# Kernel tuning notes

Measured on AMD Instinct MI355X. Metric: run time of the kernel, lower is better.

Reference implementation:

```python
import jax, jax.numpy as jnp
import numpy as np

BASE_DIM = 512
NUM_HEADS = 4
HEAD_DIM = BASE_DIM // NUM_HEADS
NUM_USERS = 100000
TIMESLOTS = 24
B, S = 64, 512


def setup_inputs() -> dict:
    key = jax.random.key(0)
    ks = jax.random.split(key, 16)
    timeslot_embedded = jax.random.normal(ks[0], (TIMESLOTS, BASE_DIM), jnp.float32)
    smoothed_timeslot_embedded = jax.random.normal(ks[1], (TIMESLOTS, BASE_DIM), jnp.float32)
    user_embedded = jax.random.normal(ks[2], (B, BASE_DIM), jnp.float32)
    user_x = jax.random.randint(ks[3], (B,), 0, NUM_USERS)
    hour_x = jax.random.randint(ks[4], (B, S), 0, TIMESLOTS)
    hour_mask = jax.random.randint(ks[5], (B, S, TIMESLOTS), 0, 2)
    # guarantee no row is fully masked (avoids all -inf softmax rows)
    hour_mask = hour_mask.at[:, :, 0].set(0)
    sc = 0.02
    user_pref_table = jax.random.normal(ks[6], (NUM_USERS, BASE_DIM), jnp.float32) * sc
    Wq = jax.random.normal(ks[7], (NUM_HEADS, HEAD_DIM, 2 * BASE_DIM), jnp.float32) * sc
    bq = jnp.zeros((NUM_HEADS, HEAD_DIM), jnp.float32)
    Wk = jax.random.normal(ks[8], (NUM_HEADS, HEAD_DIM, BASE_DIM), jnp.float32) * sc
    bk = jnp.zeros((NUM_HEADS, HEAD_DIM), jnp.float32)
    Wv = jax.random.normal(ks[9], (NUM_HEADS, HEAD_DIM, BASE_DIM), jnp.float32) * sc
    bv = jnp.zeros((NUM_HEADS, HEAD_DIM), jnp.float32)
    W_unify = jax.random.normal(ks[10], (BASE_DIM, BASE_DIM), jnp.float32) * sc
    b_unify = jnp.zeros((BASE_DIM,), jnp.float32)
    W_time = jax.random.normal(ks[11], (TIMESLOTS, BASE_DIM), jnp.float32) * sc
    b_time = jnp.zeros((TIMESLOTS,), jnp.float32)
    return dict(timeslot_embedded=timeslot_embedded,
                smoothed_timeslot_embedded=smoothed_timeslot_embedded,
                user_embedded=user_embedded,
                user_x=user_x, hour_x=hour_x, hour_mask=hour_mask,
                user_pref_table=user_pref_table,
                Wq=Wq, bq=bq, Wk=Wk, bk=bk, Wv=Wv, bv=bv,
                W_unify=W_unify, b_unify=b_unify,
                W_time=W_time, b_time=b_time)


def reference(timeslot_embedded, smoothed_timeslot_embedded, user_embedded,
              user_x, hour_x, hour_mask, user_pref_table,
              Wq, bq, Wk, bk, Wv, bv, W_unify, b_unify, W_time, b_time):
    b, s = hour_x.shape
    n = b * s
    hour = hour_x.reshape(n)                                  # [N]
    mask = hour_mask.reshape(n, TIMESLOTS)                    # [N, 24]

    # user preference broadcast over sequence, then flattened
    up = user_pref_table[user_x]                              # [B, D]
    user_feature = jnp.broadcast_to(up[:, None, :], (b, s, BASE_DIM)).reshape(n, BASE_DIM)
    time_feature = timeslot_embedded[hour]                    # [N, D]
    query = jnp.concatenate([user_feature, time_feature], axis=-1)  # [N, 2D]

    # all heads batched (equivalent to the per-head Python loop + concat)
    q = jnp.einsum('nd,hed->nhe', query, Wq) + bq             # [N, H, E]
    k = jnp.einsum('kd,hed->khe', timeslot_embedded, Wk) + bk # [24, H, E]
    v = jnp.einsum('kd,hed->khe', timeslot_embedded, Wv) + bv # [24, H, E]

    scale = 1.0 / jnp.sqrt(jnp.float32(HEAD_DIM))
    scores = jnp.einsum('nhe,khe->nhk', q, k) * scale         # [N, H, 24]
    scores = jnp.where(mask[:, None, :] == 1, -jnp.inf, scores)
    attn = jax.nn.softmax(scores, axis=-1)
    out = jnp.einsum('nhk,khe->nhe', attn, v).reshape(n, BASE_DIM)  # concat heads

    head_outputs = out.reshape(b, s, BASE_DIM)
    at_emb = head_outputs @ W_unify.T + b_unify               # [B, S, D]
    time_logits = head_outputs @ W_time.T + b_time            # [B, S, 24]
    return at_emb, time_logits
```

## Files before the change

### kernel.cpp

```cpp
#include <hip/hip_runtime.h>
#include <hip/hip_bf16.h>
#include <math.h>

#define TS   24
#define NH   4
#define HD   128
#define D    512
#define NB   64
#define SEQ  512
#define NTOT (NB*SEQ)

typedef __bf16 bf16;
typedef __bf16 bf16x8 __attribute__((ext_vector_type(8)));
typedef float  f32x4  __attribute__((ext_vector_type(4)));

#define OFF_QU  0
#define OFF_QT  32768
#define OFF_K   45056
#define OFF_V   57344
#define OFF_SU  69632
#define OFF_ST  75776
#define OFF_BSW 78080

__global__ __launch_bounds__(256) void k1_proj(
    const float* __restrict__ timeslot, const int* __restrict__ user_x,
    const float* __restrict__ upt,
    const float* __restrict__ Wq, const float* __restrict__ bq,
    const float* __restrict__ Wk, const float* __restrict__ bk,
    const float* __restrict__ Wv, const float* __restrict__ bv,
    float* __restrict__ ws)
{
    int tau = blockIdx.x * 256 + threadIdx.x;
    if (tau < 32768) {
        int he = tau >> 6, b = tau & 63;
        const float4* wrow = (const float4*)(Wq + (size_t)he * 1024);
        int u = user_x[b];
        const float4* urow = (const float4*)(upt + (size_t)u * 512);
        float acc = bq[he];
        #pragma unroll 4
        for (int d = 0; d < 128; ++d) {
            float4 w = wrow[d], x = urow[d];
            acc += w.x*x.x + w.y*x.y + w.z*x.z + w.w*x.w;
        }
        ws[OFF_QU + b*512 + he] = acc;
    } else if (tau < 69632) {
        int idx = tau - 32768;
        int sec = idx / 12288;
        int r   = idx % 12288;
        int he  = r / 24, t = r % 24;
        const float* wbase; float bias; int outoff;
        if (sec == 0)      { wbase = Wq + (size_t)he*1024 + 512; bias = 0.f;    outoff = OFF_QT; }
        else if (sec == 1) { wbase = Wk + (size_t)he*512;        bias = bk[he]; outoff = OFF_K;  }
        else               { wbase = Wv + (size_t)he*512;        bias = bv[he]; outoff = OFF_V;  }
        const float4* w4 = (const float4*)wbase;
        const float4* x4 = (const float4*)(timeslot + t*512);
        float acc = bias;
        #pragma unroll 4
        for (int d = 0; d < 128; ++d) {
            float4 w = w4[d], x = x4[d];
            acc += w.x*x.x + w.y*x.y + w.z*x.z + w.w*x.w;
        }
        ws[outoff + t*512 + he] = acc;
    }
}

static __device__ __forceinline__ float dot128(const float* __restrict__ a,
                                               const float* __restrict__ b) {
    const float4* a4 = (const float4*)a;
    const float4* b4 = (const float4*)b;
    float acc = 0.f;
    #pragma unroll 8
    for (int i = 0; i < 32; ++i) {
        float4 x = a4[i], y = b4[i];
        acc += x.x*y.x + x.y*y.y + x.z*y.z + x.w*y.w;
    }
    return acc;
}

__global__ __launch_bounds__(256) void k2_small(
    const float* __restrict__ Wu, const float* __restrict__ Wt,
    float* __restrict__ ws)
{
    const float SCL = 1.4426950408889634f / sqrtf(128.0f);
    int tau = blockIdx.x * 256 + threadIdx.x;
    bf16* Bsw = (bf16*)(ws + OFF_BSW);
    if (tau < 6144) {
        int kk = tau % 24, h = (tau / 24) & 3, b = tau / 96;
        float acc = dot128(ws + OFF_QU + b*512 + h*128, ws + OFF_K + kk*512 + h*128);
        ws[OFF_SU + tau] = acc * SCL;
    } else if (tau < 8448) {
        int i = tau - 6144;
        int kk = i % 24, h = (i / 24) & 3, t = i / 96;
        float acc = dot128(ws + OFF_QT + t*512 + h*128, ws + OFF_K + kk*512 + h*128);
        ws[OFF_ST + i] = acc * SCL;
    } else if (tau < 57600) {
        int i = tau - 8448;
        int c = i & 511, r96 = i >> 9;
        int h = r96 / 24, kk = r96 % 24;
        float acc = dot128(ws + OFF_V + kk*512 + h*128, Wu + (size_t)c*512 + h*128);
        Bsw[((r96 >> 3)*544 + c)*8 + (r96 & 7)] = (bf16)acc;
    } else if (tau < 59904) {
        int i = tau - 57600;
        int j = i % 24, r96 = i / 24;
        int h = r96 / 24, kk = r96 % 24;
        float acc = dot128(ws + OFF_V + kk*512 + h*128, Wt + (size_t)j*512 + h*128);
        Bsw[((r96 >> 3)*544 + 512 + j)*8 + (r96 & 7)] = (bf16)acc;
    } else if (tau < 60672) {
        int i = tau - 59904;
        int g = i >> 6, rem = i & 63;
        int c = 536 + (rem >> 3), j = rem & 7;
        Bsw[(g*544 + c)*8 + j] = (bf16)0.f;
    }
}

__global__ __launch_bounds__(256) void k3_main(
    const int* __restrict__ hour_x, const int* __restrict__ hour_mask,
    const float* __restrict__ b_unify, const float* __restrict__ b_time,
    const float* __restrict__ ws, float* __restrict__ out)
{
    __shared__ int  maskL[128 * 24];
    __shared__ int  hourL[128];
    __shared__ __align__(16) bf16 attnL[128][104];

    int tid = threadIdx.x;
    int n0  = blockIdx.x * 128;
    int b   = n0 >> 9;

    {
        const int4* src = (const int4*)(hour_mask + (size_t)n0 * 24);
        int4* dst = (int4*)maskL;
        #pragma unroll
        for (int i = tid; i < 128 * 24 / 4; i += 256)
            dst[i] = src[i];
        if (tid < 128) hourL[tid] = hour_x[n0 + tid];
    }
    __syncthreads();

    #pragma unroll
    for (int it = 0; it < 2; ++it) {
        int task = tid + it * 256;
        int h = task >> 7, row = task & 127;
        int t = hourL[row];
        const float* su = ws + OFF_SU + (b*4 + h)*24;
        const float* st = ws + OFF_ST + (t*4 + h)*24;
        const int*   m  = maskL + row*24;
        float w[24]; float sum = 0.f;
        #pragma unroll
        for (int kk = 0; kk < 24; ++kk) {
            float e = exp2f(su[kk] + st[kk]);
            e = m[kk] ? 0.f : e;
            w[kk] = e; sum += e;
        }
        float inv = 1.f / sum;
        #pragma unroll
        for (int kk = 0; kk < 24; ++kk)
            attnL[row][h*24 + kk] = (bf16)(w[kk] * inv);
    }
    __syncthreads();

    const bf16* Bsw = (const bf16*)(ws + OFF_BSW);
    int wv = tid >> 6, l = tid & 63;
    int quad = l >> 4, cl = l & 15;
    int r0 = wv*32 + cl;
    int r1 = r0 + 16;

    bf16x8 a00 = *(const bf16x8*)&attnL[r0][ 0 + quad*8];
    bf16x8 a01 = *(const bf16x8*)&attnL[r0][32 + quad*8];
    bf16x8 a02 = *(const bf16x8*)&attnL[r0][64 + quad*8];
    bf16x8 a10 = *(const bf16x8*)&attnL[r1][ 0 + quad*8];
    bf16x8 a11 = *(const bf16x8*)&attnL[r1][32 + quad*8];
    bf16x8 a12 = *(const bf16x8*)&attnL[r1][64 + quad*8];

    int nbase = n0 + wv*32 + quad*4;

    for (int ct = 0; ct < 32; ++ct) {
        int col = ct*16 + cl;
        const bf16* bp = Bsw + ((size_t)(quad*544 + col)) * 8;
        bf16x8 b0 = *(const bf16x8*)(bp);
        bf16x8 b1 = *(const bf16x8*)(bp + 4*544*8);
        bf16x8 b2 = *(const bf16x8*)(bp + 8*544*8);
        f32x4 acc0 = {0.f, 0.f, 0.f, 0.f};
        f32x4 acc1 = {0.f, 0.f, 0.f, 0.f};
        acc0 = __builtin_amdgcn_mfma_f32_16x16x32_bf16(a00, b0, acc0, 0, 0, 0);
        acc1 = __builtin_amdgcn_mfma_f32_16x16x32_bf16(a10, b0, acc1, 0, 0, 0);
        acc0 = __builtin_amdgcn_mfma_f32_16x16x32_bf16(a01, b1, acc0, 0, 0, 0);
        acc1 = __builtin_amdgcn_mfma_f32_16x16x32_bf16(a11, b1, acc1, 0, 0, 0);
        acc0 = __builtin_amdgcn_mfma_f32_16x16x32_bf16(a02, b2, acc0, 0, 0, 0);
        acc1 = __builtin_amdgcn_mfma_f32_16x16x32_bf16(a12, b2, acc1, 0, 0, 0);
        float bias = b_unify[col];
        #pragma unroll
        for (int r = 0; r < 4; ++r) {
            out[(size_t)(nbase + r)*512 + col]      = acc0[r] + bias;
            out[(size_t)(nbase + 16 + r)*512 + col] = acc1[r] + bias;
        }
    }

    float* tl_out = out + (size_t)NTOT * 512;
    for (int ct = 32; ct < 34; ++ct) {
        int col = ct*16 + cl;
        int cc  = col - 512;
        const bf16* bp = Bsw + ((size_t)(quad*544 + col)) * 8;
        bf16x8 b0 = *(const bf16x8*)(bp);
        bf16x8 b1 = *(const bf16x8*)(bp + 4*544*8);
        bf16x8 b2 = *(const bf16x8*)(bp + 8*544*8);
        f32x4 acc0 = {0.f, 0.f, 0.f, 0.f};
        f32x4 acc1 = {0.f, 0.f, 0.f, 0.f};
        acc0 = __builtin_amdgcn_mfma_f32_16x16x32_bf16(a00, b0, acc0, 0, 0, 0);
        acc1 = __builtin_amdgcn_mfma_f32_16x16x32_bf16(a10, b0, acc1, 0, 0, 0);
        acc0 = __builtin_amdgcn_mfma_f32_16x16x32_bf16(a01, b1, acc0, 0, 0, 0);
        acc1 = __builtin_amdgcn_mfma_f32_16x16x32_bf16(a11, b1, acc1, 0, 0, 0);
        acc0 = __builtin_amdgcn_mfma_f32_16x16x32_bf16(a02, b2, acc0, 0, 0, 0);
        acc1 = __builtin_amdgcn_mfma_f32_16x16x32_bf16(a12, b2, acc1, 0, 0, 0);
        if (cc < 24) {
            float bias = b_time[cc];
            #pragma unroll
            for (int r = 0; r < 4; ++r) {
                tl_out[(size_t)(nbase + r)*24 + cc]      = acc0[r] + bias;
                tl_out[(size_t)(nbase + 16 + r)*24 + cc] = acc1[r] + bias;
            }
        }
    }
}

extern "C" void kernel_launch(void* const* d_in, const int* in_sizes, int n_in,
                              void* d_out, int out_size, void* d_ws, size_t ws_size,
                              hipStream_t stream) {
    const float* timeslot = (const float*)d_in[0];
    const int*   user_x   = (const int*)d_in[3];
    const int*   hour_x   = (const int*)d_in[4];
    const int*   hour_mask= (const int*)d_in[5];
    const float* upt      = (const float*)d_in[6];
    const float* Wq       = (const float*)d_in[7];
    const float* bq       = (const float*)d_in[8];
    const float* Wk       = (const float*)d_in[9];
    const float* bk       = (const float*)d_in[10];
    const float* Wv       = (const float*)d_in[11];
    const float* bv       = (const float*)d_in[12];
    const float* Wu       = (const float*)d_in[13];
    const float* b_unify  = (const float*)d_in[14];
    const float* Wt       = (const float*)d_in[15];
    const float* b_time   = (const float*)d_in[16];

    float* ws  = (float*)d_ws;
    float* out = (float*)d_out;

    k1_proj <<<272, 256, 0, stream>>>(timeslot, user_x, upt, Wq, bq, Wk, bk, Wv, bv, ws);
    k2_small<<<237, 256, 0, stream>>>(Wu, Wt, ws);
    k3_main <<<256, 256, 0, stream>>>(hour_x, hour_mask, b_unify, b_time, ws, out);
}
```

Before: 345.5 us.

## Split projection dot products across four lanes and widen main kernel blocks

The k1 and k2 precompute kernels now give each output to four threads. Each thread computes a quarter of the dot product, and the partial sums are combined with cross-lane shuffles, giving four times as many threads with shorter serial loops. k3 moves to 512-thread blocks where each wave handles 16 rows instead of 32, which raises the wave count per block. The trade-off is that each B fragment loaded in k3 now feeds half as many MFMAs, so per-row B reads rise, and the precompute grids grow with many idle lanes at store time.

```diff
diff --git a/kernel.cpp b/kernel.cpp
--- a/kernel.cpp
+++ b/kernel.cpp
@@ -21,6 +21,19 @@
 #define OFF_SU  69632
 #define OFF_ST  75776
 #define OFF_BSW 78080
+
+static __device__ __forceinline__ float dot32(const float* __restrict__ a,
+                                              const float* __restrict__ b) {
+    const float4* a4 = (const float4*)a;
+    const float4* b4 = (const float4*)b;
+    float acc = 0.f;
+    #pragma unroll
+    for (int i = 0; i < 8; ++i) {
+        float4 x = a4[i], y = b4[i];
+        acc += x.x*y.x + x.y*y.y + x.z*y.z + x.w*y.w;
+    }
+    return acc;
+}
 
 __global__ __launch_bounds__(256) void k1_proj(
     const float* __restrict__ timeslot, const int* __restrict__ user_x,
@@ -30,21 +43,24 @@
     const float* __restrict__ Wv, const float* __restrict__ bv,
     float* __restrict__ ws)
 {
-    int tau = blockIdx.x * 256 + threadIdx.x;
-    if (tau < 32768) {
-        int he = tau >> 6, b = tau & 63;
-        const float4* wrow = (const float4*)(Wq + (size_t)he * 1024);
+    int gid = blockIdx.x * 256 + threadIdx.x;
+    int o = gid >> 2, q = gid & 3;
+    if (o < 32768) {
+        int he = o >> 6, b = o & 63;
+        const float4* wrow = (const float4*)(Wq + (size_t)he * 1024) + q*32;
         int u = user_x[b];
-        const float4* urow = (const float4*)(upt + (size_t)u * 512);
-        float acc = bq[he];
-        #pragma unroll 4
-        for (int d = 0; d < 128; ++d) {
+        const float4* urow = (const float4*)(upt + (size_t)u * 512) + q*32;
+        float acc = 0.f;
+        #pragma unroll 8
+        for (int d = 0; d < 32; ++d) {
             float4 w = wrow[d], x = urow[d];
             acc += w.x*x.x + w.y*x.y + w.z*x.z + w.w*x.w;
         }
-        ws[OFF_QU + b*512 + he] = acc;
-    } else if (tau < 69632) {
-        int idx = tau - 32768;
+        acc += __shfl_xor(acc, 1);
+        acc += __shfl_xor(acc, 2);
+        if (q == 0) ws[OFF_QU + b*512 + he] = acc + bq[he];
+    } else {
+        int idx = o - 32768;
         int sec = idx / 12288;
         int r   = idx % 12288;
         int he  = r / 24, t = r % 24;
@@ -52,29 +68,18 @@
         if (sec == 0)      { wbase = Wq + (size_t)he*1024 + 512; bias = 0.f;    outoff = OFF_QT; }
         else if (sec == 1) { wbase = Wk + (size_t)he*512;        bias = bk[he]; outoff = OFF_K;  }
         else               { wbase = Wv + (size_t)he*512;        bias = bv[he]; outoff = OFF_V;  }
-        const float4* w4 = (const float4*)wbase;
-        const float4* x4 = (const float4*)(timeslot + t*512);
-        float acc = bias;
-        #pragma unroll 4
-        for (int d = 0; d < 128; ++d) {
+        const float4* w4 = (const float4*)wbase + q*32;
+        const float4* x4 = (const float4*)(timeslot + t*512) + q*32;
+        float acc = 0.f;
+        #pragma unroll 8
+        for (int d = 0; d < 32; ++d) {
             float4 w = w4[d], x = x4[d];
             acc += w.x*x.x + w.y*x.y + w.z*x.z + w.w*x.w;
         }
-        ws[outoff + t*512 + he] = acc;
-    }
-}
-
-static __device__ __forceinline__ float dot128(const float* __restrict__ a,
-                                               const float* __restrict__ b) {
-    const float4* a4 = (const float4*)a;
-    const float4* b4 = (const float4*)b;
-    float acc = 0.f;
-    #pragma unroll 8
-    for (int i = 0; i < 32; ++i) {
-        float4 x = a4[i], y = b4[i];
-        acc += x.x*y.x + x.y*y.y + x.z*y.z + x.w*y.w;
-    }
-    return acc;
+        acc += __shfl_xor(acc, 1);
+        acc += __shfl_xor(acc, 2);
+        if (q == 0) ws[outoff + t*512 + he] = acc + bias;
+    }
 }
 
 __global__ __launch_bounds__(256) void k2_small(
@@ -82,38 +87,52 @@
     float* __restrict__ ws)
 {
     const float SCL = 1.4426950408889634f / sqrtf(128.0f);
-    int tau = blockIdx.x * 256 + threadIdx.x;
+    int gid = blockIdx.x * 256 + threadIdx.x;
+    int o = gid >> 2, q = gid & 3;
+    int qo = q * 32;
     bf16* Bsw = (bf16*)(ws + OFF_BSW);
-    if (tau < 6144) {
-        int kk = tau % 24, h = (tau / 24) & 3, b = tau / 96;
-        float acc = dot128(ws + OFF_QU + b*512 + h*128, ws + OFF_K + kk*512 + h*128);
-        ws[OFF_SU + tau] = acc * SCL;
-    } else if (tau < 8448) {
-        int i = tau - 6144;
+    if (o < 6144) {
+        int kk = o % 24, h = (o / 24) & 3, b = o / 96;
+        float acc = dot32(ws + OFF_QU + b*512 + h*128 + qo,
+                          ws + OFF_K  + kk*512 + h*128 + qo);
+        acc += __shfl_xor(acc, 1);
+        acc += __shfl_xor(acc, 2);
+        if (q == 0) ws[OFF_SU + o] = acc * SCL;
+    } else if (o < 8448) {
+        int i = o - 6144;
         int kk = i % 24, h = (i / 24) & 3, t = i / 96;
-        float acc = dot128(ws + OFF_QT + t*512 + h*128, ws + OFF_K + kk*512 + h*128);
-        ws[OFF_ST + i] = acc * SCL;
-    } else if (tau < 57600) {
-        int i = tau - 8448;
+        float acc = dot32(ws + OFF_QT + t*512 + h*128 + qo,
+                          ws + OFF_K  + kk*512 + h*128 + qo);
+        acc += __shfl_xor(acc, 1);
+        acc += __shfl_xor(acc, 2);
+        if (q == 0) ws[OFF_ST + i] = acc * SCL;
+    } else if (o < 57600) {
+        int i = o - 8448;
         int c = i & 511, r96 = i >> 9;
         int h = r96 / 24, kk = r96 % 24;
-        float acc = dot128(ws + OFF_V + kk*512 + h*128, Wu + (size_t)c*512 + h*128);
-        Bsw[((r96 >> 3)*544 + c)*8 + (r96 & 7)] = (bf16)acc;
-    } else if (tau < 59904) {
-        int i = tau - 57600;
+        float acc = dot32(ws + OFF_V + kk*512 + h*128 + qo,
+                          Wu + (size_t)c*512 + h*128 + qo);
+        acc += __shfl_xor(acc, 1);
+        acc += __shfl_xor(acc, 2);
+        if (q == 0) Bsw[((r96 >> 3)*544 + c)*8 + (r96 & 7)] = (bf16)acc;
+    } else if (o < 59904) {
+        int i = o - 57600;
         int j = i % 24, r96 = i / 24;
         int h = r96 / 24, kk = r96 % 24;
-        float acc = dot128(ws + OFF_V + kk*512 + h*128, Wt + (size_t)j*512 + h*128);
-        Bsw[((r96 >> 3)*544 + 512 + j)*8 + (r96 & 7)] = (bf16)acc;
-    } else if (tau < 60672) {
-        int i = tau - 59904;
-        int g = i >> 6, rem = i & 63;
+        float acc = dot32(ws + OFF_V + kk*512 + h*128 + qo,
+                          Wt + (size_t)j*512 + h*128 + qo);
+        acc += __shfl_xor(acc, 1);
+        acc += __shfl_xor(acc, 2);
+        if (q == 0) Bsw[((r96 >> 3)*544 + 512 + j)*8 + (r96 & 7)] = (bf16)acc;
+    } else {
+        int i = o - 59904;
+        int grp = i >> 6, rem = i & 63;
         int c = 536 + (rem >> 3), j = rem & 7;
-        Bsw[(g*544 + c)*8 + j] = (bf16)0.f;
-    }
-}
-
-__global__ __launch_bounds__(256) void k3_main(
+        if (q == 0) Bsw[(grp*544 + c)*8 + j] = (bf16)0.f;
+    }
+}
+
+__global__ __launch_bounds__(512) void k3_main(
     const int* __restrict__ hour_x, const int* __restrict__ hour_mask,
     const float* __restrict__ b_unify, const float* __restrict__ b_time,
     const float* __restrict__ ws, float* __restrict__ out)
@@ -129,17 +148,14 @@
     {
         const int4* src = (const int4*)(hour_mask + (size_t)n0 * 24);
         int4* dst = (int4*)maskL;
-        #pragma unroll
-        for (int i = tid; i < 128 * 24 / 4; i += 256)
+        for (int i = tid; i < 128 * 24 / 4; i += 512)
             dst[i] = src[i];
         if (tid < 128) hourL[tid] = hour_x[n0 + tid];
     }
     __syncthreads();
 
-    #pragma unroll
-    for (int it = 0; it < 2; ++it) {
-        int task = tid + it * 256;
-        int h = task >> 7, row = task & 127;
+    {
+        int h = tid >> 7, row = tid & 127;
         int t = hourL[row];
         const float* su = ws + OFF_SU + (b*4 + h)*24;
         const float* st = ws + OFF_ST + (t*4 + h)*24;
@@ -161,17 +177,13 @@
     const bf16* Bsw = (const bf16*)(ws + OFF_BSW);
     int wv = tid >> 6, l = tid & 63;
     int quad = l >> 4, cl = l & 15;
-    int r0 = wv*32 + cl;
-    int r1 = r0 + 16;
-
-    bf16x8 a00 = *(const bf16x8*)&attnL[r0][ 0 + quad*8];
-    bf16x8 a01 = *(const bf16x8*)&attnL[r0][32 + quad*8];
-    bf16x8 a02 = *(const bf16x8*)&attnL[r0][64 + quad*8];
-    bf16x8 a10 = *(const bf16x8*)&attnL[r1][ 0 + quad*8];
-    bf16x8 a11 = *(const bf16x8*)&attnL[r1][32 + quad*8];
-    bf16x8 a12 = *(const bf16x8*)&attnL[r1][64 + quad*8];
-
-    int nbase = n0 + wv*32 + quad*4;
+    int r0 = wv*16 + cl;
+
+    bf16x8 a0 = *(const bf16x8*)&attnL[r0][ 0 + quad*8];
+    bf16x8 a1 = *(const bf16x8*)&attnL[r0][32 + quad*8];
+    bf16x8 a2 = *(const bf16x8*)&attnL[r0][64 + quad*8];
+
+    int nbase = n0 + wv*16 + quad*4;
 
     for (int ct = 0; ct < 32; ++ct) {
         int col = ct*16 + cl;
@@ -179,20 +191,14 @@
         bf16x8 b0 = *(const bf16x8*)(bp);
         bf16x8 b1 = *(const bf16x8*)(bp + 4*544*8);
         bf16x8 b2 = *(const bf16x8*)(bp + 8*544*8);
-        f32x4 acc0 = {0.f, 0.f, 0.f, 0.f};
-        f32x4 acc1 = {0.f, 0.f, 0.f, 0.f};
-        acc0 = __builtin_amdgcn_mfma_f32_16x16x32_bf16(a00, b0, acc0, 0, 0, 0);
-        acc1 = __builtin_amdgcn_mfma_f32_16x16x32_bf16(a10, b0, acc1, 0, 0, 0);
-        acc0 = __builtin_amdgcn_mfma_f32_16x16x32_bf16(a01, b1, acc0, 0, 0, 0);
-        acc1 = __builtin_amdgcn_mfma_f32_16x16x32_bf16(a11, b1, acc1, 0, 0, 0);
-        acc0 = __builtin_amdgcn_mfma_f32_16x16x32_bf16(a02, b2, acc0, 0, 0, 0);
-        acc1 = __builtin_amdgcn_mfma_f32_16x16x32_bf16(a12, b2, acc1, 0, 0, 0);
+        f32x4 acc = {0.f, 0.f, 0.f, 0.f};
+        acc = __builtin_amdgcn_mfma_f32_16x16x32_bf16(a0, b0, acc, 0, 0, 0);
+        acc = __builtin_amdgcn_mfma_f32_16x16x32_bf16(a1, b1, acc, 0, 0, 0);
+        acc = __builtin_amdgcn_mfma_f32_16x16x32_bf16(a2, b2, acc, 0, 0, 0);
         float bias = b_unify[col];
         #pragma unroll
-        for (int r = 0; r < 4; ++r) {
-            out[(size_t)(nbase + r)*512 + col]      = acc0[r] + bias;
-            out[(size_t)(nbase + 16 + r)*512 + col] = acc1[r] + bias;
-        }
+        for (int r = 0; r < 4; ++r)
+            out[(size_t)(nbase + r)*512 + col] = acc[r] + bias;
     }
 
     float* tl_out = out + (size_t)NTOT * 512;
@@ -203,21 +209,15 @@
         bf16x8 b0 = *(const bf16x8*)(bp);
         bf16x8 b1 = *(const bf16x8*)(bp + 4*544*8);
         bf16x8 b2 = *(const bf16x8*)(bp + 8*544*8);
-        f32x4 acc0 = {0.f, 0.f, 0.f, 0.f};
-        f32x4 acc1 = {0.f, 0.f, 0.f, 0.f};
-        acc0 = __builtin_amdgcn_mfma_f32_16x16x32_bf16(a00, b0, acc0, 0, 0, 0);
-        acc1 = __builtin_amdgcn_mfma_f32_16x16x32_bf16(a10, b0, acc1, 0, 0, 0);
-        acc0 = __builtin_amdgcn_mfma_f32_16x16x32_bf16(a01, b1, acc0, 0, 0, 0);
-        acc1 = __builtin_amdgcn_mfma_f32_16x16x32_bf16(a11, b1, acc1, 0, 0, 0);
-        acc0 = __builtin_amdgcn_mfma_f32_16x16x32_bf16(a02, b2, acc0, 0, 0, 0);
-        acc1 = __builtin_amdgcn_mfma_f32_16x16x32_bf16(a12, b2, acc1, 0, 0, 0);
+        f32x4 acc = {0.f, 0.f, 0.f, 0.f};
+        acc = __builtin_amdgcn_mfma_f32_16x16x32_bf16(a0, b0, acc, 0, 0, 0);
+        acc = __builtin_amdgcn_mfma_f32_16x16x32_bf16(a1, b1, acc, 0, 0, 0);
+        acc = __builtin_amdgcn_mfma_f32_16x16x32_bf16(a2, b2, acc, 0, 0, 0);
         if (cc < 24) {
             float bias = b_time[cc];
             #pragma unroll
-            for (int r = 0; r < 4; ++r) {
-                tl_out[(size_t)(nbase + r)*24 + cc]      = acc0[r] + bias;
-                tl_out[(size_t)(nbase + 16 + r)*24 + cc] = acc1[r] + bias;
-            }
+            for (int r = 0; r < 4; ++r)
+                tl_out[(size_t)(nbase + r)*24 + cc] = acc[r] + bias;
         }
     }
 }
@@ -244,7 +244,7 @@
     float* ws  = (float*)d_ws;
     float* out = (float*)d_out;
 
-    k1_proj <<<272, 256, 0, stream>>>(timeslot, user_x, upt, Wq, bq, Wk, bk, Wv, bv, ws);
-    k2_small<<<237, 256, 0, stream>>>(Wu, Wt, ws);
-    k3_main <<<256, 256, 0, stream>>>(hour_x, hour_mask, b_unify, b_time, ws, out);
-}
+    k1_proj <<<1088, 256, 0, stream>>>(timeslot, user_x, upt, Wq, bq, Wk, bk, Wv, bv, ws);
+    k2_small<<<948,  256, 0, stream>>>(Wu, Wt, ws);
+    k3_main <<<256,  512, 0, stream>>>(hour_x, hour_mask, b_unify, b_time, ws, out);
+}
```

Measured after the change: 348.8 us. About the same (+1.0%).
